# Performance work log

Hardware: AMD Instinct MI355X
Metric: run time of the kernel (lower is better)

## Reference

```python
import jax, jax.numpy as jnp
import numpy as np
from math import sqrt

B, H, S, D = 4, 16, 2048, 64
NEG = -1000000000.0

def setup_inputs() -> dict:
    key = jax.random.key(0)
    kq, kk, kv, km = jax.random.split(key, 4)
    Q = jax.random.normal(kq, (B, H, S, D), dtype=jnp.float32)
    K = jax.random.normal(kk, (B, H, S, D), dtype=jnp.float32)
    V = jax.random.normal(kv, (B, H, S, D), dtype=jnp.float32)
    mask = jax.random.uniform(km, (B, 1, S, S)) < 0.1
    return {"Q": Q, "K": K, "V": V, "mask": mask}

def reference(Q, K, V, mask) -> jnp.ndarray:
    # scores: [B,H,S,S]
    scores = jnp.einsum('bhqd,bhkd->bhqk', Q, K)
    scores = jnp.where(mask, NEG, scores)
    attn = jax.nn.softmax(scores / sqrt(Q.shape[-1]), axis=-1)
    return jnp.einsum('bhqk,bhkd->bhqd', attn, V)
```

## Files before the change

kernel.cpp:

```cpp
#include <hip/hip_runtime.h>


#define SEQ 2048
#define DIM 64
#define NBH 64
#define LOG2E 1.44269504088896340736f
#define SCL (0.125f * LOG2E)
#define NEG_SCALED -1.25e8f

typedef short bf16x8 __attribute__((ext_vector_type(8)));
typedef float f32x4 __attribute__((ext_vector_type(4)));
typedef float f32x16 __attribute__((ext_vector_type(16)));

static __device__ __forceinline__ unsigned short f2bf(float f) {
    unsigned int u = __float_as_uint(f);
    u += 0x7fffu + ((u >> 16) & 1u);
    return (unsigned short)(u >> 16);
}

__global__ __launch_bounds__(256)
void prep_all_kernel(const float* __restrict__ K, const float* __restrict__ V,
                     const int* __restrict__ M,
                     unsigned short* __restrict__ Fb, unsigned int* __restrict__ Mpt) {
    const int x = blockIdx.x;
    const int t = threadIdx.x;
    if (x < 1024) {
        __shared__ unsigned int Wt[64][8];
        const int m  = x;
        const int b  = m >> 8;
        const int q0 = ((m >> 3) & 31) * 64;
        const int k0 = (m & 7) * 256;
        const int w  = t >> 6, l = t & 63;
        #pragma unroll 4
        for (int row = 0; row < 16; ++row) {
            const int q = q0 + w * 16 + row;
            int4 v4 = *(const int4*)(M + ((size_t)b * SEQ + q) * SEQ + k0 + l * 4);
            unsigned int nib = (unsigned int)(v4.x != 0) | ((unsigned int)(v4.y != 0) << 1)
                             | ((unsigned int)(v4.z != 0) << 2) | ((unsigned int)(v4.w != 0) << 3);
            unsigned int v = nib << (4 * (l & 7));
            v |= __shfl_xor(v, 1);
            v |= __shfl_xor(v, 2);
            v |= __shfl_xor(v, 4);
            if ((l & 7) == 0) Wt[w * 16 + row][l >> 3] = v;
        }
        __syncthreads();
        {
            const int q = t & 63, g0 = t >> 6;
            #pragma unroll
            for (int gg = 0; gg < 2; ++gg) {
                const int g = g0 + gg * 4;
                Mpt[((size_t)b * 64 + (k0 >> 5) + g) * SEQ + q0 + q] = Wt[q][g];
            }
        }
    } else if (x < 3072) {
        const int kb = x - 1024;
        const int bh = kb >> 5;
        const int g  = kb & 31;
        const float* Kg = K + ((size_t)bh * SEQ + g * 64) * DIM;
        unsigned short* Fo = Fb + (((size_t)bh * 32 + g) * 8192);
        #pragma unroll
        for (int i = 0; i < 2; ++i) {
            const int u   = i * 256 + t;
            const int sub = u >> 8;
            const int dc  = (u >> 6) & 3;
            const int ln  = u & 63;
            const int hh  = ln >> 5;
            const int q32 = ln & 31;
            const float* kp = Kg + (size_t)(sub * 32 + q32) * DIM + dc * 16 + hh * 8;
            float4 a = *(const float4*)kp;
            float4 b2 = *(const float4*)(kp + 4);
            union { uint4 q4; unsigned short s[8]; } w;
            w.s[0] = f2bf(a.x); w.s[1] = f2bf(a.y); w.s[2] = f2bf(a.z); w.s[3] = f2bf(a.w);
            w.s[4] = f2bf(b2.x); w.s[5] = f2bf(b2.y); w.s[6] = f2bf(b2.z); w.s[7] = f2bf(b2.w);
            *(uint4*)(Fo + (size_t)u * 8) = w.q4;
        }
    } else {
        __shared__ __align__(16) unsigned short T[64 * 64];
        const int vb = x - 3072;
        const int bh = vb >> 5;
        const int g  = vb & 31;
        const int k0 = g * 64;
        {
            const float* Vb = V + ((size_t)bh * SEQ + k0) * DIM;
            #pragma unroll
            for (int j = 0; j < 4; ++j) {
                const int fi = (j * 256 + t) * 4;
                const int kk = fi >> 6;
                const int d0 = fi & 63;
                float4 f = *(const float4*)(Vb + fi);
                const int u  = (kk & ~12) | ((kk & 4) << 1) | ((kk & 8) >> 1);
                const int cs = (d0 >> 4) ^ ((u >> 3) & 3);
                union { uint2 q; unsigned short s[4]; } w4;
                w4.s[0] = f2bf(f.x); w4.s[1] = f2bf(f.y);
                w4.s[2] = f2bf(f.z); w4.s[3] = f2bf(f.w);
                *(uint2*)&T[u * 64 + cs * 16 + (d0 & 15)] = w4.q;
            }
        }
        __syncthreads();
        {
            const int p   = t & 31;
            const int w2  = t >> 5;
            const int sub = w2 >> 2;
            const int kk  = (w2 >> 1) & 1;
            const int hh  = w2 & 1;
            const int dh  = p >> 4;
            const int q32a = (2 * p) & 31;
            const int ub  = sub * 32 + kk * 16 + hh * 8;
            const unsigned int* T32 = (const unsigned int*)T;
            union { uint4 q4; unsigned short s[8]; } o0, o1;
            #pragma unroll
            for (int j = 0; j < 8; ++j) {
                const int u  = ub + j;
                const int ch = (p >> 3) ^ ((u >> 3) & 3);
                unsigned int v = T32[u * 32 + ch * 8 + (p & 7)];
                o0.s[j] = (unsigned short)v;
                o1.s[j] = (unsigned short)(v >> 16);
            }
            unsigned short* dst = Fb + (((size_t)bh * 32 + g) * 8192) + 4096
                                + sub * 2048 + kk * 1024 + dh * 512 + hh * 256 + q32a * 8;
            *(uint4*)dst       = o0.q4;
            *(uint4*)(dst + 8) = o1.q4;
        }
    }
}


#define LDFRAG(fr4, bp)                                                         \
    { fr4[0] = *(const bf16x8*)(bp);                                            \
      fr4[1] = *(const bf16x8*)((bp) + 512);                                    \
      fr4[2] = *(const bf16x8*)((bp) + 1024);                                   \
      fr4[3] = *(const bf16x8*)((bp) + 1536); }

#define TILE_QK_R(sc, kf, mwv)                                                  \
    {                                                                           \
        const unsigned int mq_ = (mwv) >> sh4;                                  \
        _Pragma("unroll")                                                       \
        for (int r = 0; r < 16; ++r) {                                          \
            const int s_ = (r & 3) + 8 * (r >> 2);                              \
            sc[r] = __int_as_float(__builtin_amdgcn_sbfe(mq_, s_, 1) & 0xC2C80000u); \
        }                                                                       \
        __builtin_amdgcn_s_setprio(1);                                          \
        _Pragma("unroll")                                                       \
        for (int dc = 0; dc < 4; ++dc)                                          \
            sc = __builtin_amdgcn_mfma_f32_32x32x16_bf16(kf[dc], qf[dc], sc, 0, 0, 0); \
        __builtin_amdgcn_s_setprio(0);                                          \
    }

#define TILE_SMPV_R(sc, vf)                                                     \
    {                                                                           \
        float pv_[16];                                                          \
        _Pragma("unroll")                                                       \
        for (int r = 0; r < 16; ++r) pv_[r] = __builtin_amdgcn_exp2f(sc[r]);    \
        _Pragma("unroll")                                                       \
        for (int r = 0; r < 16; r += 4) {                                       \
            ls0 += pv_[r + 0]; ls1 += pv_[r + 1];                               \
            ls2 += pv_[r + 2]; ls3 += pv_[r + 3];                               \
        }                                                                       \
        unsigned int pk_[8];                                                    \
        _Pragma("unroll")                                                       \
        for (int m = 0; m < 8; ++m)                                             \
            asm("v_cvt_pk_bf16_f32 %0, %1, %2"                                  \
                : "=v"(pk_[m]) : "v"(pv_[2 * m]), "v"(pv_[2 * m + 1]));         \
        __builtin_amdgcn_s_setprio(1);                                          \
        _Pragma("unroll")                                                       \
        for (int kk = 0; kk < 2; ++kk) {                                        \
            union { unsigned int u[4]; bf16x8 v; } fr;                          \
            fr.u[0] = pk_[4 * kk + 0]; fr.u[1] = pk_[4 * kk + 1];               \
            fr.u[2] = pk_[4 * kk + 2]; fr.u[3] = pk_[4 * kk + 3];               \
            acc[0] = __builtin_amdgcn_mfma_f32_32x32x16_bf16(vf[kk * 2 + 0], fr.v, acc[0], 0, 0, 0); \
            acc[1] = __builtin_amdgcn_mfma_f32_32x32x16_bf16(vf[kk * 2 + 1], fr.v, acc[1], 0, 0, 0); \
        }                                                                       \
        __builtin_amdgcn_s_setprio(0);                                          \
    }

__global__ __launch_bounds__(128, 3)
void attn_main_kernel(const float* __restrict__ Q,
                      const unsigned short* __restrict__ Fb,
                      const unsigned int* __restrict__ Mpt,
                      float* __restrict__ O)
{
    const int n    = blockIdx.x;
    const int mI   = n >> 3;
    const int bh   = (n & 7) * 8 + (mI >> 5);
    const int qc   = mI & 31;
    const int b    = bh >> 4;
    const int tid  = threadIdx.x;
    const int wave = tid >> 6;
    const int lane = tid & 63;
    const int h    = lane >> 5;
    const int q32  = lane & 31;
    const int sh4  = 4 * h;
    const int q0   = qc * 64 + wave * 32;

    bf16x8 qf[4];
    {
        const float* qp = Q + ((size_t)bh * SEQ + q0 + q32) * DIM + h * 8;
        #pragma unroll
        for (int dc = 0; dc < 4; ++dc) {
            float4 xx = *(const float4*)(qp + dc * 16);
            float4 yy = *(const float4*)(qp + dc * 16 + 4);
            qf[dc][0] = (short)f2bf(xx.x * SCL); qf[dc][1] = (short)f2bf(xx.y * SCL);
            qf[dc][2] = (short)f2bf(xx.z * SCL); qf[dc][3] = (short)f2bf(xx.w * SCL);
            qf[dc][4] = (short)f2bf(yy.x * SCL); qf[dc][5] = (short)f2bf(yy.y * SCL);
            qf[dc][6] = (short)f2bf(yy.z * SCL); qf[dc][7] = (short)f2bf(yy.w * SCL);
        }
    }

    const unsigned short* pG = Fb + (size_t)bh * 32 * 8192 + lane * 8;
    const unsigned int* mr = Mpt + (size_t)b * 64 * SEQ + (q0 + q32);

    f32x16 acc[2];
    #pragma unroll
    for (int i = 0; i < 16; ++i) { acc[0][i] = 0.f; acc[1][i] = 0.f; }
    float ls0 = 0.f, ls1 = 0.f, ls2 = 0.f, ls3 = 0.f;

    bf16x8 kA[4], kB[4], vC[4];
    unsigned int mA, mB;

    LDFRAG(kA, pG);
    mA = mr[0];

    #pragma unroll 1
    for (int t = 0; t < 64; t += 2) {
        LDFRAG(kB, pG + 2048);
        mB = mr[SEQ];
        LDFRAG(vC, pG + 4096);
        {
            f32x16 sc;
            TILE_QK_R(sc, kA, mA);
            TILE_SMPV_R(sc, vC);
        }
        pG += 8192;
        mr += 2 * SEQ;
        if (t + 2 < 64) {
            LDFRAG(kA, pG);
            mA = mr[0];
        }
        LDFRAG(vC, pG - 2048);
        {
            f32x16 sc;
            TILE_QK_R(sc, kB, mB);
            TILE_SMPV_R(sc, vC);
        }
    }

    float lsum = (ls0 + ls1) + (ls2 + ls3);
    lsum += __shfl_xor(lsum, 32);
    const float inv = 1.f / lsum;
    float* orow = O + ((size_t)bh * SEQ + q0 + q32) * DIM;
    #pragma unroll
    for (int dh = 0; dh < 2; ++dh) {
        #pragma unroll
        for (int r23 = 0; r23 < 4; ++r23) {
            float4 w;
            w.x = acc[dh][4 * r23 + 0] * inv;
            w.y = acc[dh][4 * r23 + 1] * inv;
            w.z = acc[dh][4 * r23 + 2] * inv;
            w.w = acc[dh][4 * r23 + 3] * inv;
            *(float4*)(orow + dh * 32 + r23 * 8 + h * 4) = w;
        }
    }
}

__global__ __launch_bounds__(256)
void attn_fallback_kernel(const float* __restrict__ Q,
                          const float* __restrict__ K,
                          const float* __restrict__ V,
                          const int* __restrict__ mask,
                          float* __restrict__ O)
{
    const int bh   = blockIdx.y;
    const int b    = bh >> 4;
    const int q0   = blockIdx.x * 64;
    const int tid  = threadIdx.x;
    const int wave = tid >> 6;
    const int lane = tid & 63;
    const int quad = lane >> 4;
    const int l16  = lane & 15;

    __shared__ __align__(16) unsigned short Klds[32][72];
    __shared__ __align__(16) unsigned short VT[64][40];
    __shared__ __align__(16) unsigned short Plds[4][16][40];

    const float* Qb = Q + (size_t)bh * SEQ * DIM;
    const float* Kb = K + (size_t)bh * SEQ * DIM;
    const float* Vb = V + (size_t)bh * SEQ * DIM;
    const int*   Mb = mask + (size_t)b * SEQ * SEQ;

    const int qrow_frag = q0 + wave * 16 + l16;
    bf16x8 qf0, qf1;
    {
        const float* qp = Qb + (size_t)qrow_frag * DIM + quad * 8;
        #pragma unroll
        for (int i = 0; i < 8; ++i) {
            qf0[i] = (short)f2bf(qp[i]);
            qf1[i] = (short)f2bf(qp[32 + i]);
        }
    }

    f32x4 acc[4];
    #pragma unroll
    for (int dg = 0; dg < 4; ++dg) acc[dg] = (f32x4){0.f, 0.f, 0.f, 0.f};
    float mrowv[4] = {-INFINITY, -INFINITY, -INFINITY, -INFINITY};
    float lrow[4] = {0.f, 0.f, 0.f, 0.f};

    const int skey = tid >> 3;
    const int sd0  = (tid & 7) * 8;
    const int vkey = tid & 31;
    const int vd0  = (tid >> 5) * 8;
    const int qrow_m = q0 + wave * 16 + quad * 4;

    for (int kb = 0; kb < SEQ; kb += 32) {
        __syncthreads();
        {
            const float* kp = Kb + (size_t)(kb + skey) * DIM + sd0;
            union { uint4 u4; unsigned short s[8]; } kw;
            #pragma unroll
            for (int i = 0; i < 8; ++i) kw.s[i] = f2bf(kp[i]);
            *(uint4*)&Klds[skey][sd0] = kw.u4;
        }
        {
            const float* vp = Vb + (size_t)(kb + vkey) * DIM + vd0;
            #pragma unroll
            for (int i = 0; i < 8; ++i) VT[vd0 + i][vkey] = f2bf(vp[i]);
        }
        __syncthreads();

        f32x4 scr[2];
        scr[0] = (f32x4){0.f, 0.f, 0.f, 0.f};
        scr[1] = (f32x4){0.f, 0.f, 0.f, 0.f};
        #pragma unroll
        for (int nt = 0; nt < 2; ++nt) {
            bf16x8 kf0 = *(const bf16x8*)&Klds[nt * 16 + l16][quad * 8];
            bf16x8 kf1 = *(const bf16x8*)&Klds[nt * 16 + l16][32 + quad * 8];
            scr[nt] = __builtin_amdgcn_mfma_f32_16x16x32_bf16(qf0, kf0, scr[nt], 0, 0, 0);
            scr[nt] = __builtin_amdgcn_mfma_f32_16x16x32_bf16(qf1, kf1, scr[nt], 0, 0, 0);
        }

        float x[2][4];
        #pragma unroll
        for (int nt = 0; nt < 2; ++nt)
            #pragma unroll
            for (int r = 0; r < 4; ++r) {
                int mv = Mb[(size_t)(qrow_m + r) * SEQ + kb + nt * 16 + l16];
                x[nt][r] = mv ? NEG_SCALED : scr[nt][r] * 0.125f;
            }

        float p[2][4];
        #pragma unroll
        for (int r = 0; r < 4; ++r) {
            float rm = fmaxf(x[0][r], x[1][r]);
            #pragma unroll
            for (int off = 1; off < 16; off <<= 1)
                rm = fmaxf(rm, __shfl_xor(rm, off, 16));
            float mn = fmaxf(mrowv[r], rm);
            float alpha = exp2f((mrowv[r] - mn) * LOG2E);
            mrowv[r] = mn;
            float p0 = exp2f((x[0][r] - mn) * LOG2E);
            float p1 = exp2f((x[1][r] - mn) * LOG2E);
            p[0][r] = p0; p[1][r] = p1;
            float rs = p0 + p1;
            #pragma unroll
            for (int off = 1; off < 16; off <<= 1)
                rs += __shfl_xor(rs, off, 16);
            lrow[r] = lrow[r] * alpha + rs;
            #pragma unroll
            for (int dg = 0; dg < 4; ++dg)
                acc[dg][r] *= alpha;
        }

        #pragma unroll
        for (int nt = 0; nt < 2; ++nt)
            #pragma unroll
            for (int r = 0; r < 4; ++r)
                Plds[wave][quad * 4 + r][nt * 16 + l16] = f2bf(p[nt][r]);

        bf16x8 pf = *(const bf16x8*)&Plds[wave][l16][quad * 8];

        #pragma unroll
        for (int dg = 0; dg < 4; ++dg) {
            bf16x8 vf = *(const bf16x8*)&VT[dg * 16 + l16][quad * 8];
            acc[dg] = __builtin_amdgcn_mfma_f32_16x16x32_bf16(pf, vf, acc[dg], 0, 0, 0);
        }
    }

    float* Ob = O + (size_t)bh * SEQ * DIM;
    #pragma unroll
    for (int r = 0; r < 4; ++r) {
        float inv = 1.f / lrow[r];
        #pragma unroll
        for (int dg = 0; dg < 4; ++dg)
            Ob[(size_t)(qrow_m + r) * DIM + dg * 16 + l16] = acc[dg][r] * inv;
    }
}

extern "C" void kernel_launch(void* const* d_in, const int* in_sizes, int n_in,
                              void* d_out, int out_size, void* d_ws, size_t ws_size,
                              hipStream_t stream) {
    const float* Q = (const float*)d_in[0];
    const float* K = (const float*)d_in[1];
    const float* V = (const float*)d_in[2];
    const int* mask = (const int*)d_in[3];
    float*        O = (float*)d_out;

    const size_t szF = (size_t)NBH * 32 * 8192 * 2;
    const size_t szM = (size_t)4 * SEQ * (SEQ / 32) * 4;
    const size_t need = szF + szM;

    if (ws_size >= need) {
        unsigned short* Fb = (unsigned short*)d_ws;
        unsigned int*  Mpt = (unsigned int*)((char*)d_ws + szF);

        prep_all_kernel<<<dim3(5120), 256, 0, stream>>>(K, V, mask, Fb, Mpt);
        attn_main_kernel<<<dim3(2048), 128, 0, stream>>>(Q, Fb, Mpt, O);
    } else {
        attn_fallback_kernel<<<dim3(SEQ / 64, NBH), 256, 0, stream>>>(Q, K, V, mask, O);
    }
}
```

Baseline: 283.4 us.

## Share K/V tiles via LDS across 8 waves with split-KV and combine

```diff
diff --git a/kernel.cpp b/kernel.cpp
--- a/kernel.cpp
+++ b/kernel.cpp
@@ -17,6 +17,10 @@
     u += 0x7fffu + ((u >> 16) & 1u);
     return (unsigned short)(u >> 16);
 }
+
+#define GLD16(gp, lp) __builtin_amdgcn_global_load_lds( \
+    (const __attribute__((address_space(1))) unsigned int*)(gp), \
+    (__attribute__((address_space(3))) unsigned int*)(lp), 16, 0, 0)
 
 __global__ __launch_bounds__(256)
 void prep_all_kernel(const float* __restrict__ K, const float* __restrict__ V,
@@ -125,55 +129,7 @@
 }
 
 
-#define LDFRAG(fr4, bp)                                                         \
-    { fr4[0] = *(const bf16x8*)(bp);                                            \
-      fr4[1] = *(const bf16x8*)((bp) + 512);                                    \
-      fr4[2] = *(const bf16x8*)((bp) + 1024);                                   \
-      fr4[3] = *(const bf16x8*)((bp) + 1536); }
-
-#define TILE_QK_R(sc, kf, mwv)                                                  \
-    {                                                                           \
-        const unsigned int mq_ = (mwv) >> sh4;                                  \
-        _Pragma("unroll")                                                       \
-        for (int r = 0; r < 16; ++r) {                                          \
-            const int s_ = (r & 3) + 8 * (r >> 2);                              \
-            sc[r] = __int_as_float(__builtin_amdgcn_sbfe(mq_, s_, 1) & 0xC2C80000u); \
-        }                                                                       \
-        __builtin_amdgcn_s_setprio(1);                                          \
-        _Pragma("unroll")                                                       \
-        for (int dc = 0; dc < 4; ++dc)                                          \
-            sc = __builtin_amdgcn_mfma_f32_32x32x16_bf16(kf[dc], qf[dc], sc, 0, 0, 0); \
-        __builtin_amdgcn_s_setprio(0);                                          \
-    }
-
-#define TILE_SMPV_R(sc, vf)                                                     \
-    {                                                                           \
-        float pv_[16];                                                          \
-        _Pragma("unroll")                                                       \
-        for (int r = 0; r < 16; ++r) pv_[r] = __builtin_amdgcn_exp2f(sc[r]);    \
-        _Pragma("unroll")                                                       \
-        for (int r = 0; r < 16; r += 4) {                                       \
-            ls0 += pv_[r + 0]; ls1 += pv_[r + 1];                               \
-            ls2 += pv_[r + 2]; ls3 += pv_[r + 3];                               \
-        }                                                                       \
-        unsigned int pk_[8];                                                    \
-        _Pragma("unroll")                                                       \
-        for (int m = 0; m < 8; ++m)                                             \
-            asm("v_cvt_pk_bf16_f32 %0, %1, %2"                                  \
-                : "=v"(pk_[m]) : "v"(pv_[2 * m]), "v"(pv_[2 * m + 1]));         \
-        __builtin_amdgcn_s_setprio(1);                                          \
-        _Pragma("unroll")                                                       \
-        for (int kk = 0; kk < 2; ++kk) {                                        \
-            union { unsigned int u[4]; bf16x8 v; } fr;                          \
-            fr.u[0] = pk_[4 * kk + 0]; fr.u[1] = pk_[4 * kk + 1];               \
-            fr.u[2] = pk_[4 * kk + 2]; fr.u[3] = pk_[4 * kk + 3];               \
-            acc[0] = __builtin_amdgcn_mfma_f32_32x32x16_bf16(vf[kk * 2 + 0], fr.v, acc[0], 0, 0, 0); \
-            acc[1] = __builtin_amdgcn_mfma_f32_32x32x16_bf16(vf[kk * 2 + 1], fr.v, acc[1], 0, 0, 0); \
-        }                                                                       \
-        __builtin_amdgcn_s_setprio(0);                                          \
-    }
-
-__global__ __launch_bounds__(128, 3)
+__global__ __launch_bounds__(512, 8)
 void attn_main_kernel(const float* __restrict__ Q,
                       const unsigned short* __restrict__ Fb,
                       const unsigned int* __restrict__ Mpt,
@@ -181,16 +137,23 @@
 {
     const int n    = blockIdx.x;
     const int mI   = n >> 3;
-    const int bh   = (n & 7) * 8 + (mI >> 5);
-    const int qc   = mI & 31;
+    const int bh   = (n & 7) * 8 + (mI >> 4);
+    const int qb   = mI & 15;
     const int b    = bh >> 4;
     const int tid  = threadIdx.x;
     const int wave = tid >> 6;
+    const int wv   = wave & 3;
+    const int c    = wave >> 2;
     const int lane = tid & 63;
     const int h    = lane >> 5;
     const int q32  = lane & 31;
     const int sh4  = 4 * h;
-    const int q0   = qc * 64 + wave * 32;
+    const int q0   = qb * 128 + wv * 32;
+
+    __shared__ __align__(16) char SmRaw[33792];
+    typedef unsigned short BlobT[2][4096];
+    BlobT* Blb = reinterpret_cast<BlobT*>(SmRaw);
+    float (*Cmb)[64][33] = reinterpret_cast<float(*)[64][33]>(SmRaw);
 
     bf16x8 qf[4];
     {
@@ -206,58 +169,117 @@
         }
     }
 
-    const unsigned short* pG = Fb + (size_t)bh * 32 * 8192 + lane * 8;
-    const unsigned int* mr = Mpt + (size_t)b * 64 * SEQ + (q0 + q32);
+    const unsigned short* Fbh = Fb + (size_t)bh * 32 * 8192;
+    const unsigned int* mp = Mpt + (size_t)b * 64 * SEQ + (q0 + q32);
 
     f32x16 acc[2];
     #pragma unroll
     for (int i = 0; i < 16; ++i) { acc[0][i] = 0.f; acc[1][i] = 0.f; }
     float ls0 = 0.f, ls1 = 0.f, ls2 = 0.f, ls3 = 0.f;
 
-    bf16x8 kA[4], kB[4], vC[4];
-    unsigned int mA, mB;
-
-    LDFRAG(kA, pG);
-    mA = mr[0];
+    {
+        const unsigned short* sb = Fbh + (size_t)(c * 16) * 8192 + wv * 512 + lane * 8;
+        GLD16(sb,        &Blb[0][c][wv * 512 + lane * 8]);
+        GLD16(sb + 4096, &Blb[0][c][2048 + wv * 512 + lane * 8]);
+    }
+    unsigned int mw = mp[(size_t)(c * 32) * SEQ];
 
     #pragma unroll 1
-    for (int t = 0; t < 64; t += 2) {
-        LDFRAG(kB, pG + 2048);
-        mB = mr[SEQ];
-        LDFRAG(vC, pG + 4096);
-        {
-            f32x16 sc;
-            TILE_QK_R(sc, kA, mA);
-            TILE_SMPV_R(sc, vC);
-        }
-        pG += 8192;
-        mr += 2 * SEQ;
-        if (t + 2 < 64) {
-            LDFRAG(kA, pG);
-            mA = mr[0];
-        }
-        LDFRAG(vC, pG - 2048);
-        {
-            f32x16 sc;
-            TILE_QK_R(sc, kB, mB);
-            TILE_SMPV_R(sc, vC);
-        }
+    for (int gp = 0; gp < 32; ++gp) {
+        __syncthreads();
+
+        unsigned int mwn = 0;
+        if (gp + 1 < 32) {
+            const int s = c * 32 + gp + 1;
+            const unsigned short* sb = Fbh + (size_t)(s >> 1) * 8192
+                                     + (size_t)(s & 1) * 2048 + wv * 512 + lane * 8;
+            const int nb = (gp + 1) & 1;
+            GLD16(sb,        &Blb[nb][c][wv * 512 + lane * 8]);
+            GLD16(sb + 4096, &Blb[nb][c][2048 + wv * 512 + lane * 8]);
+            mwn = mp[(size_t)s * SEQ];
+        }
+
+        const unsigned short* Bl = &Blb[gp & 1][c][0] + lane * 8;
+
+        const unsigned int mq = mw >> sh4;
+        f32x16 sc;
+        #pragma unroll
+        for (int r = 0; r < 16; ++r) {
+            const int s_ = (r & 3) + 8 * (r >> 2);
+            sc[r] = __int_as_float(__builtin_amdgcn_sbfe(mq, s_, 1) & 0xC2C80000u);
+        }
+        __builtin_amdgcn_s_setprio(1);
+        #pragma unroll
+        for (int dc = 0; dc < 4; ++dc) {
+            bf16x8 kf = *(const bf16x8*)(Bl + dc * 512);
+            sc = __builtin_amdgcn_mfma_f32_32x32x16_bf16(kf, qf[dc], sc, 0, 0, 0);
+        }
+        __builtin_amdgcn_s_setprio(0);
+
+        float pv[16];
+        #pragma unroll
+        for (int r = 0; r < 16; ++r) pv[r] = __builtin_amdgcn_exp2f(sc[r]);
+        #pragma unroll
+        for (int r = 0; r < 16; r += 4) {
+            ls0 += pv[r + 0]; ls1 += pv[r + 1];
+            ls2 += pv[r + 2]; ls3 += pv[r + 3];
+        }
+        unsigned int pk[8];
+        #pragma unroll
+        for (int m = 0; m < 8; ++m)
+            asm("v_cvt_pk_bf16_f32 %0, %1, %2"
+                : "=v"(pk[m]) : "v"(pv[2 * m]), "v"(pv[2 * m + 1]));
+
+        __builtin_amdgcn_s_setprio(1);
+        #pragma unroll
+        for (int kk = 0; kk < 2; ++kk) {
+            union { unsigned int u[4]; bf16x8 v; } fr;
+            fr.u[0] = pk[4 * kk + 0]; fr.u[1] = pk[4 * kk + 1];
+            fr.u[2] = pk[4 * kk + 2]; fr.u[3] = pk[4 * kk + 3];
+            #pragma unroll
+            for (int dh = 0; dh < 2; ++dh) {
+                bf16x8 vf = *(const bf16x8*)(Bl + 2048 + kk * 1024 + dh * 512);
+                acc[dh] = __builtin_amdgcn_mfma_f32_32x32x16_bf16(vf, fr.v, acc[dh], 0, 0, 0);
+            }
+        }
+        __builtin_amdgcn_s_setprio(0);
+
+        mw = mwn;
     }
 
     float lsum = (ls0 + ls1) + (ls2 + ls3);
-    lsum += __shfl_xor(lsum, 32);
-    const float inv = 1.f / lsum;
-    float* orow = O + ((size_t)bh * SEQ + q0 + q32) * DIM;
-    #pragma unroll
-    for (int dh = 0; dh < 2; ++dh) {
-        #pragma unroll
-        for (int r23 = 0; r23 < 4; ++r23) {
-            float4 w;
-            w.x = acc[dh][4 * r23 + 0] * inv;
-            w.y = acc[dh][4 * r23 + 1] * inv;
-            w.z = acc[dh][4 * r23 + 2] * inv;
-            w.w = acc[dh][4 * r23 + 3] * inv;
-            *(float4*)(orow + dh * 32 + r23 * 8 + h * 4) = w;
+    __syncthreads();
+    if (c == 1) {
+        #pragma unroll
+        for (int i = 0; i < 16; ++i) {
+            Cmb[wv][lane][i]      = acc[0][i];
+            Cmb[wv][lane][16 + i] = acc[1][i];
+        }
+        Cmb[wv][lane][32] = lsum;
+    }
+    __syncthreads();
+    if (c == 0) {
+        #pragma unroll
+        for (int i = 0; i < 16; ++i) {
+            acc[0][i] += Cmb[wv][lane][i];
+            acc[1][i] += Cmb[wv][lane][16 + i];
+        }
+        lsum += Cmb[wv][lane][32];
+
+        lsum += __shfl_xor(lsum, 32);
+        const float inv = 1.f / lsum;
+        float* orow = O + ((size_t)bh * SEQ + q0 + q32) * DIM;
+        #pragma unroll
+        for (int dh = 0; dh < 2; ++dh) {
+            #pragma unroll
+            for (int r23 = 0; r23 < 4; ++r23) {
+                float4 w;
+                w.x = acc[dh][4 * r23 + 0] * inv;
+                w.y = acc[dh][4 * r23 + 1] * inv;
+                w.z = acc[dh][4 * r23 + 2] * inv;
+                w.w = acc[dh][4 * r23 + 3] * inv;
+                *(float4*)(orow + dh * 32 + r23 * 8 + h * 4) = w;
+            }
         }
     }
 }
@@ -412,7 +434,7 @@
         unsigned int*  Mpt = (unsigned int*)((char*)d_ws + szF);
 
         prep_all_kernel<<<dim3(5120), 256, 0, stream>>>(K, V, mask, Fb, Mpt);
-        attn_main_kernel<<<dim3(2048), 128, 0, stream>>>(Q, Fb, Mpt, O);
+        attn_main_kernel<<<dim3(1024), 512, 0, stream>>>(Q, Fb, Mpt, O);
     } else {
         attn_fallback_kernel<<<dim3(SEQ / 64, NBH), 256, 0, stream>>>(Q, K, V, mask, O);
     }
```

New measurement: 564.6 us. +99.3%, slower.
